# Kernel tuning notes

Hardware: AMD Instinct MI355X
Metric: run time of the kernel (lower is better)

## Reference

```python
import jax, jax.numpy as jnp
import numpy as np


def setup_inputs() -> dict:
    key = jax.random.key(0)
    k1, k2, k3, k4 = jax.random.split(key, 4)
    N, K, P2 = 4096, 256, 96  # examples, freqs, 2*p
    z = jax.random.normal(k1, (N, K, P2), dtype=jnp.float32)
    sigma_1 = jax.random.normal(k2, (K, P2, P2), dtype=jnp.float32)
    sigma_2 = jax.random.normal(k3, (K, P2, P2), dtype=jnp.float32)
    weights = jax.random.normal(k4, (K, P2, P2), dtype=jnp.float32)
    return {"z": z, "sigma_1": sigma_1, "sigma_2": sigma_2,
            "weights": weights, "n_1": 500, "n_2": 400}


def reference(z, sigma_1, sigma_2, weights, n_1, n_2):
    # z: (N, K, 2p), weights/sigma_1: (K, 2p, 2p)
    P2 = z.shape[-1]
    const = jnp.log(jnp.float32(n_1) / jnp.float32(n_2))
    # quadratic form z^T W_j z, batched over (example, freq)
    quad = jnp.einsum('nfp,fpq,nfq->nf', z, weights, z)  # (N, K)
    # det(W_j @ Sigma1_j + I) per frequency (independent of example)
    A = jnp.matmul(weights, sigma_1) + jnp.eye(P2, dtype=z.dtype)  # (K, 2p, 2p)
    det = jnp.clip(jnp.linalg.det(A), 1e-5, 1e5)  # (K,)
    sum_freq = quad - jnp.log(det)[None, :]  # (N, K)
    out = sum_freq.sum(axis=-1) + const  # (N,)
    return out.reshape(-1, 1)
```

## Files before the change

### kernel.cpp

```cpp
#include <hip/hip_runtime.h>


typedef __attribute__((ext_vector_type(8))) short bf16x8;
typedef __attribute__((ext_vector_type(4))) float f32x4;

#define WFENCE() asm volatile("" ::: "memory")

__device__ __forceinline__ unsigned short f2bf(float x) {
  unsigned int u = __builtin_bit_cast(unsigned int, x);
  u += 0x7fffu + ((u >> 16) & 1u);
  return (unsigned short)(u >> 16);
}
__device__ __forceinline__ float bf2f(unsigned short h) {
  unsigned int u = ((unsigned int)h) << 16;
  return __builtin_bit_cast(float, u);
}

#define ALD 100
#define WLD 35
#define ZLD 104

__device__ __forceinline__ void det_body(const int lane, const int f,
                                         const float* __restrict__ W,
                                         const float* __restrict__ S1,
                                         float* __restrict__ logdet,
                                         float* smem) {
  float* Wc = smem;
  float* Sc = smem + 3360;
  float* Al = smem;

  const float* Wg = W + (size_t)f * 9216;
  const float* Sg = S1 + (size_t)f * 9216;

  const int i0 = (lane >> 3) * 12;
  const int j0 = (lane & 7) * 12;

  float acc[12][12];
#pragma unroll
  for (int a = 0; a < 12; ++a)
#pragma unroll
    for (int b = 0; b < 12; ++b) acc[a][b] = 0.f;

  for (int kc = 0; kc < 3; ++kc) {
#pragma unroll
    for (int it = 0; it < 12; ++it) {
      int c = lane + it * 64;
      int i = c >> 3;
      int k4 = (c & 7) << 2;
      const float4 v =
          *reinterpret_cast<const float4*>(Wg + i * 96 + kc * 32 + k4);
      Wc[i * WLD + k4 + 0] = v.x;
      Wc[i * WLD + k4 + 1] = v.y;
      Wc[i * WLD + k4 + 2] = v.z;
      Wc[i * WLD + k4 + 3] = v.w;
    }
#pragma unroll
    for (int it = 0; it < 12; ++it) {
      int c = lane + it * 64;
      int kk = c / 24;
      int j4 = (c % 24) << 2;
      const float4 v =
          *reinterpret_cast<const float4*>(Sg + (kc * 32 + kk) * 96 + j4);
      *reinterpret_cast<float4*>(&Sc[kk * 100 + j4]) = v;
    }
    WFENCE();
#pragma unroll 2
    for (int kk = 0; kk < 32; ++kk) {
      float wv[12];
#pragma unroll
      for (int r = 0; r < 12; ++r) wv[r] = Wc[(i0 + r) * WLD + kk];
      float sv[12];
      const float4 s0 = *reinterpret_cast<const float4*>(&Sc[kk * 100 + j0]);
      const float4 s1 =
          *reinterpret_cast<const float4*>(&Sc[kk * 100 + j0 + 4]);
      const float4 s2 =
          *reinterpret_cast<const float4*>(&Sc[kk * 100 + j0 + 8]);
      sv[0] = s0.x; sv[1] = s0.y; sv[2] = s0.z; sv[3] = s0.w;
      sv[4] = s1.x; sv[5] = s1.y; sv[6] = s1.z; sv[7] = s1.w;
      sv[8] = s2.x; sv[9] = s2.y; sv[10] = s2.z; sv[11] = s2.w;
#pragma unroll
      for (int a = 0; a < 12; ++a)
#pragma unroll
        for (int b = 0; b < 12; ++b) acc[a][b] += wv[a] * sv[b];
    }
    WFENCE();
  }

#pragma unroll
  for (int a = 0; a < 12; ++a) {
    int i = i0 + a;
#pragma unroll
    for (int c4 = 0; c4 < 3; ++c4) {
      float4 v;
      v.x = acc[a][c4 * 4 + 0] + ((i == j0 + c4 * 4 + 0) ? 1.f : 0.f);
      v.y = acc[a][c4 * 4 + 1] + ((i == j0 + c4 * 4 + 1) ? 1.f : 0.f);
      v.z = acc[a][c4 * 4 + 2] + ((i == j0 + c4 * 4 + 2) ? 1.f : 0.f);
      v.w = acc[a][c4 * 4 + 3] + ((i == j0 + c4 * 4 + 3) ? 1.f : 0.f);
      *reinterpret_cast<float4*>(&Al[i * ALD + j0 + c4 * 4]) = v;
    }
  }
  WFENCE();

  float ls = 0.f;
  int neg = 0;
  int sgn = 0;

  for (int p = 0; p < 12; ++p) {
    const int c0 = p * 8;
    const int NC = 88 - c0;
    const int NT = NC >> 2;
    const bool e0 = lane <= 95 - c0;
    const bool e1 = (c0 < 32) && (lane <= 31 - c0);

    float P0[8], P1[8];
#pragma unroll
    for (int m = 0; m < 8; ++m) { P0[m] = 0.f; P1[m] = 0.f; }
    if (e0) {
      const float4 x =
          *reinterpret_cast<const float4*>(&Al[(c0 + lane) * ALD + c0]);
      const float4 y =
          *reinterpret_cast<const float4*>(&Al[(c0 + lane) * ALD + c0 + 4]);
      P0[0] = x.x; P0[1] = x.y; P0[2] = x.z; P0[3] = x.w;
      P0[4] = y.x; P0[5] = y.y; P0[6] = y.z; P0[7] = y.w;
    }
    if (e1) {
      const float4 x =
          *reinterpret_cast<const float4*>(&Al[(c0 + 64 + lane) * ALD + c0]);
      const float4 y =
          *reinterpret_cast<const float4*>(&Al[(c0 + 64 + lane) * ALD + c0 + 4]);
      P1[0] = x.x; P1[1] = x.y; P1[2] = x.z; P1[3] = x.w;
      P1[4] = y.x; P1[5] = y.y; P1[6] = y.z; P1[7] = y.w;
    }

#pragma unroll
    for (int j = 0; j < 8; ++j) {
      const int jc = c0 + j;
      float pv;
      int tried = 0;
      for (;;) {
        pv = __shfl(P0[j], j);
        if (fabsf(pv) >= 1e-3f || tried) break;
        tried = 1;
        unsigned k0 = (e0 && lane >= j)
                          ? ((__float_as_uint(fabsf(P0[j])) & ~127u) |
                             (unsigned)lane)
                          : 0u;
        unsigned k1 = e1 ? ((__float_as_uint(fabsf(P1[j])) & ~127u) | 64u |
                            (unsigned)lane)
                         : 0u;
        unsigned key = k0 > k1 ? k0 : k1;
#pragma unroll
        for (int m = 1; m < 64; m <<= 1) {
          unsigned o = (unsigned)__shfl_xor((int)key, m);
          key = key > o ? key : o;
        }
        const int wl = (int)(key & 63u);
        const int slot = (int)((key >> 6) & 1u);
        const int bi = c0 + slot * 64 + wl;
        if (bi <= jc) break;
        sgn ^= 1;
#pragma unroll
        for (int m = 0; m < 8; ++m) {
          const float vj = __shfl(P0[m], j);
          const float vb0 = __shfl(P0[m], wl);
          const float vb1 = __shfl(P1[m], wl);
          const float vb = slot ? vb1 : vb0;
          if (lane == j) P0[m] = vb;
          if (lane == wl) {
            if (slot) P1[m] = vj;
            else P0[m] = vj;
          }
        }
        if (lane < NT) {
          const int col0 = c0 + 8 + lane * 4;
          float4 xx = *reinterpret_cast<float4*>(&Al[jc * ALD + col0]);
          float4 yy = *reinterpret_cast<float4*>(&Al[bi * ALD + col0]);
          *reinterpret_cast<float4*>(&Al[jc * ALD + col0]) = yy;
          *reinterpret_cast<float4*>(&Al[bi * ALD + col0]) = xx;
        }
        WFENCE();
      }
      const float rpv = __builtin_amdgcn_rcpf(pv);
      const bool up0 = e0 && (lane > j);
      const float L0 = P0[j] * rpv;
      const float L1 = P1[j] * rpv;
      if (up0) P0[j] = L0;
      if (e1) P1[j] = L1;
#pragma unroll
      for (int jj = j + 1; jj < 8; ++jj) {
        const float u = __shfl(P0[jj], j);
        if (up0) P0[jj] -= L0 * u;
        if (e1) P1[jj] -= L1 * u;
      }
      ls += logf(fabsf(pv));
      if (pv < 0.f) neg ^= 1;
    }
    WFENCE();

    if (NC > 0) {
      const int ca = c0 + 8 + lane;
      const bool va = lane < NC;
      const int cb = ca + 64;
      const bool vb = (lane + 64) < NC;
      float a[8], b[8];
#pragma unroll
      for (int i = 0; i < 8; ++i) {
        a[i] = va ? Al[(c0 + i) * ALD + ca] : 0.f;
        b[i] = vb ? Al[(c0 + i) * ALD + cb] : 0.f;
      }
#pragma unroll
      for (int jj = 1; jj < 8; ++jj)
#pragma unroll
        for (int i = 0; i < jj; ++i) {
          const float Lv = __shfl(P0[i], jj);
          a[jj] -= Lv * a[i];
          b[jj] -= Lv * b[i];
        }
#pragma unroll
      for (int i = 0; i < 8; ++i) {
        if (va) Al[(c0 + i) * ALD + ca] = a[i];
        if (vb) Al[(c0 + i) * ALD + cb] = b[i];
      }
      WFENCE();

      const bool r0v = e0 && (lane >= 8);
      const bool r1v = e1;
      const int r0 = (c0 + lane) * ALD;
      const int r1 = (c0 + 64 + lane) * ALD;
      for (int ct = 0; ct < NT; ++ct) {
        const int col0 = c0 + 8 + ct * 4;
        float4 u[8];
#pragma unroll
        for (int i = 0; i < 8; ++i)
          u[i] = *reinterpret_cast<const float4*>(&Al[(c0 + i) * ALD + col0]);
        if (r0v) {
          float4 x = *reinterpret_cast<float4*>(&Al[r0 + col0]);
#pragma unroll
          for (int i = 0; i < 8; ++i) {
            x.x -= P0[i] * u[i].x;
            x.y -= P0[i] * u[i].y;
            x.z -= P0[i] * u[i].z;
            x.w -= P0[i] * u[i].w;
          }
          *reinterpret_cast<float4*>(&Al[r0 + col0]) = x;
        }
        if (r1v) {
          float4 x = *reinterpret_cast<float4*>(&Al[r1 + col0]);
#pragma unroll
          for (int i = 0; i < 8; ++i) {
            x.x -= P1[i] * u[i].x;
            x.y -= P1[i] * u[i].y;
            x.z -= P1[i] * u[i].z;
            x.w -= P1[i] * u[i].w;
          }
          *reinterpret_cast<float4*>(&Al[r1 + col0]) = x;
        }
      }
    }
    WFENCE();
  }

  if (lane == 0) {
    const float LMIN = -11.5129254f, LMAX = 11.5129254f;
    float c;
    if (neg ^ sgn) c = LMIN;
    else c = fminf(fmaxf(ls, LMIN), LMAX);
    logdet[f] = c;
  }
}

__device__ __forceinline__ void quad_body(const int tid, const int idx,
                                          const float* __restrict__ z,
                                          const float* __restrict__ W,
                                          float* __restrict__ partial,
                                          float* smem) {
  unsigned short* Zb = reinterpret_cast<unsigned short*>(smem);
  unsigned short* Wb = Zb + 128 * ZLD;

  const int lane = tid & 63, wave = tid >> 6;
  const int n0 = (idx & 31) * 128;
  const int f0 = (idx >> 5) * 16;
  const int lrow = lane & 15;
  const int lq = lane >> 4;
  const int lk8 = lq * 8;
  const int rgrp = tid >> 3;
  const int cgrp = tid & 7;

  float dotacc[2][4];
#pragma unroll
  for (int mt = 0; mt < 2; ++mt)
#pragma unroll
    for (int i = 0; i < 4; ++i) dotacc[mt][i] = 0.f;

  for (int ff = 0; ff < 16; ++ff) {
    const int f = f0 + ff;
#pragma unroll
    for (int p = 0; p < 4; ++p) {
      int r = p * 32 + rgrp;
      const float4* src = reinterpret_cast<const float4*>(
          z + (size_t)(n0 + r) * 24576 + (size_t)f * 96);
#pragma unroll
      for (int cc = 0; cc < 3; ++cc) {
        int c = cgrp + cc * 8;
        float4 d = src[c];
        ushort4 s;
        s.x = f2bf(d.x); s.y = f2bf(d.y); s.z = f2bf(d.z); s.w = f2bf(d.w);
        *reinterpret_cast<ushort4*>(&Zb[r * ZLD + c * 4]) = s;
      }
    }
    const float4* wsrc =
        reinterpret_cast<const float4*>(W + (size_t)f * 9216);
#pragma unroll
    for (int it = 0; it < 9; ++it) {
      int c = tid + it * 256;
      int k = c / 24, q4 = (c % 24) << 2;
      float4 d = wsrc[c];
      ushort4 s;
      s.x = f2bf(d.x); s.y = f2bf(d.y); s.z = f2bf(d.z); s.w = f2bf(d.w);
      *reinterpret_cast<ushort4*>(&Wb[k * ZLD + q4]) = s;
    }
    __syncthreads();

    f32x4 acc[2][6];
#pragma unroll
    for (int mt = 0; mt < 2; ++mt)
#pragma unroll
      for (int nt = 0; nt < 6; ++nt) acc[mt][nt] = (f32x4){0.f, 0.f, 0.f, 0.f};

#pragma unroll
    for (int ks = 0; ks < 3; ++ks) {
      bf16x8 a0 = *reinterpret_cast<const bf16x8*>(
          &Zb[(wave * 32 + lrow) * ZLD + ks * 32 + lk8]);
      bf16x8 a1 = *reinterpret_cast<const bf16x8*>(
          &Zb[(wave * 32 + 16 + lrow) * ZLD + ks * 32 + lk8]);
#pragma unroll
      for (int nt = 0; nt < 6; ++nt) {
        bf16x8 b = *reinterpret_cast<const bf16x8*>(
            &Wb[(nt * 16 + lrow) * ZLD + ks * 32 + lk8]);
        acc[0][nt] =
            __builtin_amdgcn_mfma_f32_16x16x32_bf16(a0, b, acc[0][nt], 0, 0, 0);
        acc[1][nt] =
            __builtin_amdgcn_mfma_f32_16x16x32_bf16(a1, b, acc[1][nt], 0, 0, 0);
      }
    }

#pragma unroll
    for (int mt = 0; mt < 2; ++mt) {
      int rbase = wave * 32 + mt * 16 + lq * 4;
#pragma unroll
      for (int i = 0; i < 4; ++i) {
        int row = rbase + i;
        float s = 0.f;
#pragma unroll
        for (int nt = 0; nt < 6; ++nt) {
          float zv = bf2f(Zb[row * ZLD + nt * 16 + lrow]);
          s += acc[mt][nt][i] * zv;
        }
        dotacc[mt][i] += s;
      }
    }
    __syncthreads();
  }

#pragma unroll
  for (int mt = 0; mt < 2; ++mt)
#pragma unroll
    for (int i = 0; i < 4; ++i) {
      float v = dotacc[mt][i];
      v += __shfl_xor(v, 1);
      v += __shfl_xor(v, 2);
      v += __shfl_xor(v, 4);
      v += __shfl_xor(v, 8);
      dotacc[mt][i] = v;
    }
  if (lrow == 0) {
#pragma unroll
    for (int mt = 0; mt < 2; ++mt) {
      int row = wave * 32 + mt * 16 + lq * 4;
      float4 o = {dotacc[mt][0], dotacc[mt][1], dotacc[mt][2], dotacc[mt][3]};
      *reinterpret_cast<float4*>(
          &partial[(size_t)(idx >> 5) * 4096 + n0 + row]) = o;
    }
  }
}

__global__ __launch_bounds__(256) void fused_kernel(
    const float* __restrict__ z, const float* __restrict__ W,
    const float* __restrict__ S1, float* __restrict__ partial,
    float* __restrict__ logdet) {
  __shared__ alignas(16) float smem[11648];
  if (blockIdx.x < 256) {
    if (threadIdx.x >= 64) return;
    det_body(threadIdx.x, blockIdx.x, W, S1, logdet, smem);
  } else {
    quad_body(threadIdx.x, blockIdx.x - 256, z, W, partial, smem);
  }
}

__global__ __launch_bounds__(256) void finalize_kernel(
    const float* __restrict__ partial, const float* __restrict__ logdet,
    const int* __restrict__ n1p, const int* __restrict__ n2p,
    float* __restrict__ out) {
  __shared__ float red[256];
  const int t = threadIdx.x;
  red[t] = logdet[t];
  __syncthreads();
  for (int s = 128; s > 0; s >>= 1) {
    if (t < s) red[t] += red[t + s];
    __syncthreads();
  }
  const float S = red[0];
  const int n = blockIdx.x * 256 + t;
  float acc = 0.f;
#pragma unroll
  for (int ft = 0; ft < 16; ++ft) acc += partial[ft * 4096 + n];
  const float cst = logf((float)(*n1p) / (float)(*n2p));
  out[n] = acc - S + cst;
}

extern "C" void kernel_launch(void* const* d_in, const int* in_sizes, int n_in,
                              void* d_out, int out_size, void* d_ws,
                              size_t ws_size, hipStream_t stream) {
  const float* z  = (const float*)d_in[0];
  const float* s1 = (const float*)d_in[1];
  const float* w  = (const float*)d_in[3];
  const int* n1   = (const int*)d_in[4];
  const int* n2   = (const int*)d_in[5];
  float* out      = (float*)d_out;

  char* ws = (char*)d_ws;
  float* partial = (float*)ws;
  float* logdet  = (float*)(ws + 262144);

  fused_kernel<<<dim3(768), dim3(256), 0, stream>>>(z, w, s1, partial, logdet);
  finalize_kernel<<<dim3(16), dim3(256), 0, stream>>>(partial, logdet, n1, n2,
                                                      out);
}
```

Baseline: 651.3 us.

## Spread determinant LU across all four waves and cap registers for occupancy

The determinant blocks previously ran on a single 64-lane wave. Now all 256 threads share the W·Sigma1 GEMM, the panel's triangular solve and the trailing update, with block barriers between phases and the pivot panel written back to shared memory. The quad MFMA accumulation is split into two groups of three tiles, and launch bounds request four blocks per CU, so the kernel uses fewer registers and can fit more blocks. The cost is many more __syncthreads in the LU loop and possible register spills under the tighter limit.

```diff
diff --git a/kernel.cpp b/kernel.cpp
--- a/kernel.cpp
+++ b/kernel.cpp
@@ -20,7 +20,7 @@
 #define WLD 35
 #define ZLD 104
 
-__device__ __forceinline__ void det_body(const int lane, const int f,
+__device__ __forceinline__ void det_body(const int tid, const int f,
                                          const float* __restrict__ W,
                                          const float* __restrict__ S1,
                                          float* __restrict__ logdet,
@@ -29,22 +29,23 @@
   float* Sc = smem + 3360;
   float* Al = smem;
 
+  const int lane = tid & 63;
   const float* Wg = W + (size_t)f * 9216;
   const float* Sg = S1 + (size_t)f * 9216;
 
-  const int i0 = (lane >> 3) * 12;
-  const int j0 = (lane & 7) * 12;
-
-  float acc[12][12];
-#pragma unroll
-  for (int a = 0; a < 12; ++a)
+  const int i0 = (tid >> 3) * 3;
+  const int j0 = (tid & 7) * 12;
+
+  float acc[3][12];
+#pragma unroll
+  for (int a = 0; a < 3; ++a)
 #pragma unroll
     for (int b = 0; b < 12; ++b) acc[a][b] = 0.f;
 
   for (int kc = 0; kc < 3; ++kc) {
 #pragma unroll
-    for (int it = 0; it < 12; ++it) {
-      int c = lane + it * 64;
+    for (int it = 0; it < 3; ++it) {
+      int c = tid + it * 256;
       int i = c >> 3;
       int k4 = (c & 7) << 2;
       const float4 v =
@@ -55,20 +56,20 @@
       Wc[i * WLD + k4 + 3] = v.w;
     }
 #pragma unroll
-    for (int it = 0; it < 12; ++it) {
-      int c = lane + it * 64;
+    for (int it = 0; it < 3; ++it) {
+      int c = tid + it * 256;
       int kk = c / 24;
       int j4 = (c % 24) << 2;
       const float4 v =
           *reinterpret_cast<const float4*>(Sg + (kc * 32 + kk) * 96 + j4);
       *reinterpret_cast<float4*>(&Sc[kk * 100 + j4]) = v;
     }
-    WFENCE();
+    __syncthreads();
 #pragma unroll 2
     for (int kk = 0; kk < 32; ++kk) {
-      float wv[12];
-#pragma unroll
-      for (int r = 0; r < 12; ++r) wv[r] = Wc[(i0 + r) * WLD + kk];
+      float wv[3];
+#pragma unroll
+      for (int r = 0; r < 3; ++r) wv[r] = Wc[(i0 + r) * WLD + kk];
       float sv[12];
       const float4 s0 = *reinterpret_cast<const float4*>(&Sc[kk * 100 + j0]);
       const float4 s1 =
@@ -79,15 +80,15 @@
       sv[4] = s1.x; sv[5] = s1.y; sv[6] = s1.z; sv[7] = s1.w;
       sv[8] = s2.x; sv[9] = s2.y; sv[10] = s2.z; sv[11] = s2.w;
 #pragma unroll
-      for (int a = 0; a < 12; ++a)
+      for (int a = 0; a < 3; ++a)
 #pragma unroll
         for (int b = 0; b < 12; ++b) acc[a][b] += wv[a] * sv[b];
     }
-    WFENCE();
-  }
-
-#pragma unroll
-  for (int a = 0; a < 12; ++a) {
+    __syncthreads();
+  }
+
+#pragma unroll
+  for (int a = 0; a < 3; ++a) {
     int i = i0 + a;
 #pragma unroll
     for (int c4 = 0; c4 < 3; ++c4) {
@@ -99,7 +100,7 @@
       *reinterpret_cast<float4*>(&Al[i * ALD + j0 + c4 * 4]) = v;
     }
   }
-  WFENCE();
+  __syncthreads();
 
   float ls = 0.f;
   int neg = 0;
@@ -109,158 +110,158 @@
     const int c0 = p * 8;
     const int NC = 88 - c0;
     const int NT = NC >> 2;
-    const bool e0 = lane <= 95 - c0;
-    const bool e1 = (c0 < 32) && (lane <= 31 - c0);
-
-    float P0[8], P1[8];
-#pragma unroll
-    for (int m = 0; m < 8; ++m) { P0[m] = 0.f; P1[m] = 0.f; }
-    if (e0) {
-      const float4 x =
-          *reinterpret_cast<const float4*>(&Al[(c0 + lane) * ALD + c0]);
-      const float4 y =
-          *reinterpret_cast<const float4*>(&Al[(c0 + lane) * ALD + c0 + 4]);
-      P0[0] = x.x; P0[1] = x.y; P0[2] = x.z; P0[3] = x.w;
-      P0[4] = y.x; P0[5] = y.y; P0[6] = y.z; P0[7] = y.w;
-    }
-    if (e1) {
-      const float4 x =
-          *reinterpret_cast<const float4*>(&Al[(c0 + 64 + lane) * ALD + c0]);
-      const float4 y =
-          *reinterpret_cast<const float4*>(&Al[(c0 + 64 + lane) * ALD + c0 + 4]);
-      P1[0] = x.x; P1[1] = x.y; P1[2] = x.z; P1[3] = x.w;
-      P1[4] = y.x; P1[5] = y.y; P1[6] = y.z; P1[7] = y.w;
-    }
-
-#pragma unroll
-    for (int j = 0; j < 8; ++j) {
-      const int jc = c0 + j;
-      float pv;
-      int tried = 0;
-      for (;;) {
-        pv = __shfl(P0[j], j);
-        if (fabsf(pv) >= 1e-3f || tried) break;
-        tried = 1;
-        unsigned k0 = (e0 && lane >= j)
-                          ? ((__float_as_uint(fabsf(P0[j])) & ~127u) |
-                             (unsigned)lane)
-                          : 0u;
-        unsigned k1 = e1 ? ((__float_as_uint(fabsf(P1[j])) & ~127u) | 64u |
-                            (unsigned)lane)
-                         : 0u;
-        unsigned key = k0 > k1 ? k0 : k1;
-#pragma unroll
-        for (int m = 1; m < 64; m <<= 1) {
-          unsigned o = (unsigned)__shfl_xor((int)key, m);
-          key = key > o ? key : o;
+
+    if (tid < 64) {
+      const bool e0 = lane <= 95 - c0;
+      const bool e1 = (c0 < 32) && (lane <= 31 - c0);
+      float P0[8], P1[8];
+#pragma unroll
+      for (int m = 0; m < 8; ++m) { P0[m] = 0.f; P1[m] = 0.f; }
+      if (e0) {
+        const float4 x =
+            *reinterpret_cast<const float4*>(&Al[(c0 + lane) * ALD + c0]);
+        const float4 y =
+            *reinterpret_cast<const float4*>(&Al[(c0 + lane) * ALD + c0 + 4]);
+        P0[0] = x.x; P0[1] = x.y; P0[2] = x.z; P0[3] = x.w;
+        P0[4] = y.x; P0[5] = y.y; P0[6] = y.z; P0[7] = y.w;
+      }
+      if (e1) {
+        const float4 x = *reinterpret_cast<const float4*>(
+            &Al[(c0 + 64 + lane) * ALD + c0]);
+        const float4 y = *reinterpret_cast<const float4*>(
+            &Al[(c0 + 64 + lane) * ALD + c0 + 4]);
+        P1[0] = x.x; P1[1] = x.y; P1[2] = x.z; P1[3] = x.w;
+        P1[4] = y.x; P1[5] = y.y; P1[6] = y.z; P1[7] = y.w;
+      }
+
+#pragma unroll
+      for (int j = 0; j < 8; ++j) {
+        const int jc = c0 + j;
+        float pv;
+        int tried = 0;
+        for (;;) {
+          pv = __shfl(P0[j], j);
+          if (fabsf(pv) >= 1e-3f || tried) break;
+          tried = 1;
+          unsigned k0 = (e0 && lane >= j)
+                            ? ((__float_as_uint(fabsf(P0[j])) & ~127u) |
+                               (unsigned)lane)
+                            : 0u;
+          unsigned k1 = e1 ? ((__float_as_uint(fabsf(P1[j])) & ~127u) | 64u |
+                              (unsigned)lane)
+                           : 0u;
+          unsigned key = k0 > k1 ? k0 : k1;
+#pragma unroll
+          for (int m = 1; m < 64; m <<= 1) {
+            unsigned o = (unsigned)__shfl_xor((int)key, m);
+            key = key > o ? key : o;
+          }
+          const int wl = (int)(key & 63u);
+          const int slot = (int)((key >> 6) & 1u);
+          const int bi = c0 + slot * 64 + wl;
+          if (bi <= jc) break;
+          sgn ^= 1;
+#pragma unroll
+          for (int m = 0; m < 8; ++m) {
+            const float vj = __shfl(P0[m], j);
+            const float vb0 = __shfl(P0[m], wl);
+            const float vb1 = __shfl(P1[m], wl);
+            const float vb = slot ? vb1 : vb0;
+            if (lane == j) P0[m] = vb;
+            if (lane == wl) {
+              if (slot) P1[m] = vj;
+              else P0[m] = vj;
+            }
+          }
+          if (lane < NT) {
+            const int col0 = c0 + 8 + lane * 4;
+            float4 xx = *reinterpret_cast<float4*>(&Al[jc * ALD + col0]);
+            float4 yy = *reinterpret_cast<float4*>(&Al[bi * ALD + col0]);
+            *reinterpret_cast<float4*>(&Al[jc * ALD + col0]) = yy;
+            *reinterpret_cast<float4*>(&Al[bi * ALD + col0]) = xx;
+          }
+          WFENCE();
         }
-        const int wl = (int)(key & 63u);
-        const int slot = (int)((key >> 6) & 1u);
-        const int bi = c0 + slot * 64 + wl;
-        if (bi <= jc) break;
-        sgn ^= 1;
-#pragma unroll
-        for (int m = 0; m < 8; ++m) {
-          const float vj = __shfl(P0[m], j);
-          const float vb0 = __shfl(P0[m], wl);
-          const float vb1 = __shfl(P1[m], wl);
-          const float vb = slot ? vb1 : vb0;
-          if (lane == j) P0[m] = vb;
-          if (lane == wl) {
-            if (slot) P1[m] = vj;
-            else P0[m] = vj;
-          }
+        const float rpv = __builtin_amdgcn_rcpf(pv);
+        const bool up0 = e0 && (lane > j);
+        const float L0 = P0[j] * rpv;
+        const float L1 = P1[j] * rpv;
+        if (up0) P0[j] = L0;
+        if (e1) P1[j] = L1;
+#pragma unroll
+        for (int jj = j + 1; jj < 8; ++jj) {
+          const float u = __shfl(P0[jj], j);
+          if (up0) P0[jj] -= L0 * u;
+          if (e1) P1[jj] -= L1 * u;
         }
-        if (lane < NT) {
-          const int col0 = c0 + 8 + lane * 4;
-          float4 xx = *reinterpret_cast<float4*>(&Al[jc * ALD + col0]);
-          float4 yy = *reinterpret_cast<float4*>(&Al[bi * ALD + col0]);
-          *reinterpret_cast<float4*>(&Al[jc * ALD + col0]) = yy;
-          *reinterpret_cast<float4*>(&Al[bi * ALD + col0]) = xx;
+        ls += logf(fabsf(pv));
+        if (pv < 0.f) neg ^= 1;
+      }
+      if (e0) {
+        float4 x = {P0[0], P0[1], P0[2], P0[3]};
+        float4 y = {P0[4], P0[5], P0[6], P0[7]};
+        *reinterpret_cast<float4*>(&Al[(c0 + lane) * ALD + c0]) = x;
+        *reinterpret_cast<float4*>(&Al[(c0 + lane) * ALD + c0 + 4]) = y;
+      }
+      if (e1) {
+        float4 x = {P1[0], P1[1], P1[2], P1[3]};
+        float4 y = {P1[4], P1[5], P1[6], P1[7]};
+        *reinterpret_cast<float4*>(&Al[(c0 + 64 + lane) * ALD + c0]) = x;
+        *reinterpret_cast<float4*>(&Al[(c0 + 64 + lane) * ALD + c0 + 4]) = y;
+      }
+    }
+    __syncthreads();
+
+    if (NC > 0) {
+      if (tid < NC) {
+        const int ca = c0 + 8 + tid;
+        float a[8];
+#pragma unroll
+        for (int i = 0; i < 8; ++i) a[i] = Al[(c0 + i) * ALD + ca];
+#pragma unroll
+        for (int jj = 1; jj < 8; ++jj)
+#pragma unroll
+          for (int i = 0; i < jj; ++i) {
+            const float Lv = Al[(c0 + jj) * ALD + c0 + i];
+            a[jj] -= Lv * a[i];
+          }
+#pragma unroll
+        for (int i = 0; i < 8; ++i) Al[(c0 + i) * ALD + ca] = a[i];
+      }
+      __syncthreads();
+
+      if (tid < NC) {
+        const int r = c0 + 8 + tid;
+        const float4 lx =
+            *reinterpret_cast<const float4*>(&Al[r * ALD + c0]);
+        const float4 ly =
+            *reinterpret_cast<const float4*>(&Al[r * ALD + c0 + 4]);
+        float Lr[8];
+        Lr[0] = lx.x; Lr[1] = lx.y; Lr[2] = lx.z; Lr[3] = lx.w;
+        Lr[4] = ly.x; Lr[5] = ly.y; Lr[6] = ly.z; Lr[7] = ly.w;
+        for (int ct = 0; ct < NT; ++ct) {
+          const int col0 = c0 + 8 + ct * 4;
+          float4 u[8];
+#pragma unroll
+          for (int i = 0; i < 8; ++i)
+            u[i] =
+                *reinterpret_cast<const float4*>(&Al[(c0 + i) * ALD + col0]);
+          float4 x = *reinterpret_cast<float4*>(&Al[r * ALD + col0]);
+#pragma unroll
+          for (int i = 0; i < 8; ++i) {
+            x.x -= Lr[i] * u[i].x;
+            x.y -= Lr[i] * u[i].y;
+            x.z -= Lr[i] * u[i].z;
+            x.w -= Lr[i] * u[i].w;
+          }
+          *reinterpret_cast<float4*>(&Al[r * ALD + col0]) = x;
         }
-        WFENCE();
-      }
-      const float rpv = __builtin_amdgcn_rcpf(pv);
-      const bool up0 = e0 && (lane > j);
-      const float L0 = P0[j] * rpv;
-      const float L1 = P1[j] * rpv;
-      if (up0) P0[j] = L0;
-      if (e1) P1[j] = L1;
-#pragma unroll
-      for (int jj = j + 1; jj < 8; ++jj) {
-        const float u = __shfl(P0[jj], j);
-        if (up0) P0[jj] -= L0 * u;
-        if (e1) P1[jj] -= L1 * u;
-      }
-      ls += logf(fabsf(pv));
-      if (pv < 0.f) neg ^= 1;
-    }
-    WFENCE();
-
-    if (NC > 0) {
-      const int ca = c0 + 8 + lane;
-      const bool va = lane < NC;
-      const int cb = ca + 64;
-      const bool vb = (lane + 64) < NC;
-      float a[8], b[8];
-#pragma unroll
-      for (int i = 0; i < 8; ++i) {
-        a[i] = va ? Al[(c0 + i) * ALD + ca] : 0.f;
-        b[i] = vb ? Al[(c0 + i) * ALD + cb] : 0.f;
-      }
-#pragma unroll
-      for (int jj = 1; jj < 8; ++jj)
-#pragma unroll
-        for (int i = 0; i < jj; ++i) {
-          const float Lv = __shfl(P0[i], jj);
-          a[jj] -= Lv * a[i];
-          b[jj] -= Lv * b[i];
-        }
-#pragma unroll
-      for (int i = 0; i < 8; ++i) {
-        if (va) Al[(c0 + i) * ALD + ca] = a[i];
-        if (vb) Al[(c0 + i) * ALD + cb] = b[i];
-      }
-      WFENCE();
-
-      const bool r0v = e0 && (lane >= 8);
-      const bool r1v = e1;
-      const int r0 = (c0 + lane) * ALD;
-      const int r1 = (c0 + 64 + lane) * ALD;
-      for (int ct = 0; ct < NT; ++ct) {
-        const int col0 = c0 + 8 + ct * 4;
-        float4 u[8];
-#pragma unroll
-        for (int i = 0; i < 8; ++i)
-          u[i] = *reinterpret_cast<const float4*>(&Al[(c0 + i) * ALD + col0]);
-        if (r0v) {
-          float4 x = *reinterpret_cast<float4*>(&Al[r0 + col0]);
-#pragma unroll
-          for (int i = 0; i < 8; ++i) {
-            x.x -= P0[i] * u[i].x;
-            x.y -= P0[i] * u[i].y;
-            x.z -= P0[i] * u[i].z;
-            x.w -= P0[i] * u[i].w;
-          }
-          *reinterpret_cast<float4*>(&Al[r0 + col0]) = x;
-        }
-        if (r1v) {
-          float4 x = *reinterpret_cast<float4*>(&Al[r1 + col0]);
-#pragma unroll
-          for (int i = 0; i < 8; ++i) {
-            x.x -= P1[i] * u[i].x;
-            x.y -= P1[i] * u[i].y;
-            x.z -= P1[i] * u[i].z;
-            x.w -= P1[i] * u[i].w;
-          }
-          *reinterpret_cast<float4*>(&Al[r1 + col0]) = x;
-        }
-      }
-    }
-    WFENCE();
-  }
-
-  if (lane == 0) {
+      }
+    }
+    __syncthreads();
+  }
+
+  if (tid == 0) {
     const float LMIN = -11.5129254f, LMAX = 11.5129254f;
     float c;
     if (neg ^ sgn) c = LMIN;
@@ -321,42 +322,49 @@
     }
     __syncthreads();
 
-    f32x4 acc[2][6];
-#pragma unroll
-    for (int mt = 0; mt < 2; ++mt)
-#pragma unroll
-      for (int nt = 0; nt < 6; ++nt) acc[mt][nt] = (f32x4){0.f, 0.f, 0.f, 0.f};
-
-#pragma unroll
-    for (int ks = 0; ks < 3; ++ks) {
-      bf16x8 a0 = *reinterpret_cast<const bf16x8*>(
-          &Zb[(wave * 32 + lrow) * ZLD + ks * 32 + lk8]);
-      bf16x8 a1 = *reinterpret_cast<const bf16x8*>(
-          &Zb[(wave * 32 + 16 + lrow) * ZLD + ks * 32 + lk8]);
-#pragma unroll
-      for (int nt = 0; nt < 6; ++nt) {
-        bf16x8 b = *reinterpret_cast<const bf16x8*>(
-            &Wb[(nt * 16 + lrow) * ZLD + ks * 32 + lk8]);
-        acc[0][nt] =
-            __builtin_amdgcn_mfma_f32_16x16x32_bf16(a0, b, acc[0][nt], 0, 0, 0);
-        acc[1][nt] =
-            __builtin_amdgcn_mfma_f32_16x16x32_bf16(a1, b, acc[1][nt], 0, 0, 0);
-      }
-    }
-
-#pragma unroll
-    for (int mt = 0; mt < 2; ++mt) {
-      int rbase = wave * 32 + mt * 16 + lq * 4;
-#pragma unroll
-      for (int i = 0; i < 4; ++i) {
-        int row = rbase + i;
-        float s = 0.f;
-#pragma unroll
-        for (int nt = 0; nt < 6; ++nt) {
-          float zv = bf2f(Zb[row * ZLD + nt * 16 + lrow]);
-          s += acc[mt][nt][i] * zv;
+#pragma unroll
+    for (int g = 0; g < 2; ++g) {
+      f32x4 acc[2][3];
+#pragma unroll
+      for (int mt = 0; mt < 2; ++mt)
+#pragma unroll
+        for (int n3 = 0; n3 < 3; ++n3)
+          acc[mt][n3] = (f32x4){0.f, 0.f, 0.f, 0.f};
+
+#pragma unroll
+      for (int ks = 0; ks < 3; ++ks) {
+        bf16x8 a0 = *reinterpret_cast<const bf16x8*>(
+            &Zb[(wave * 32 + lrow) * ZLD + ks * 32 + lk8]);
+        bf16x8 a1 = *reinterpret_cast<const bf16x8*>(
+            &Zb[(wave * 32 + 16 + lrow) * ZLD + ks * 32 + lk8]);
+#pragma unroll
+        for (int n3 = 0; n3 < 3; ++n3) {
+          const int nt = g * 3 + n3;
+          bf16x8 b = *reinterpret_cast<const bf16x8*>(
+              &Wb[(nt * 16 + lrow) * ZLD + ks * 32 + lk8]);
+          acc[0][n3] = __builtin_amdgcn_mfma_f32_16x16x32_bf16(a0, b,
+                                                              acc[0][n3],
+                                                              0, 0, 0);
+          acc[1][n3] = __builtin_amdgcn_mfma_f32_16x16x32_bf16(a1, b,
+                                                              acc[1][n3],
+                                                              0, 0, 0);
         }
-        dotacc[mt][i] += s;
+      }
+
+#pragma unroll
+      for (int mt = 0; mt < 2; ++mt) {
+        int rbase = wave * 32 + mt * 16 + lq * 4;
+#pragma unroll
+        for (int i = 0; i < 4; ++i) {
+          int row = rbase + i;
+          float s = 0.f;
+#pragma unroll
+          for (int n3 = 0; n3 < 3; ++n3) {
+            float zv = bf2f(Zb[row * ZLD + (g * 3 + n3) * 16 + lrow]);
+            s += acc[mt][n3][i] * zv;
+          }
+          dotacc[mt][i] += s;
+        }
       }
     }
     __syncthreads();
@@ -384,13 +392,12 @@
   }
 }
 
-__global__ __launch_bounds__(256) void fused_kernel(
+__global__ __launch_bounds__(256, 4) void fused_kernel(
     const float* __restrict__ z, const float* __restrict__ W,
     const float* __restrict__ S1, float* __restrict__ partial,
     float* __restrict__ logdet) {
   __shared__ alignas(16) float smem[11648];
   if (blockIdx.x < 256) {
-    if (threadIdx.x >= 64) return;
     det_body(threadIdx.x, blockIdx.x, W, S1, logdet, smem);
   } else {
     quad_body(threadIdx.x, blockIdx.x - 256, z, W, partial, smem);
```

New measurement: 634.0 us. 2.7% less time.
